# Optimization experiments

Measured on AMD Instinct MI355X. Metric: run time of the kernel, lower is better.

## Reference

```python
import jax, jax.numpy as jnp
import numpy as np

B, L, D, H, PD = 4, 8192, 512, 8, 1
DK = D // H
EPS = 1e-5


def setup_inputs() -> dict:
    root = jax.random.key(0)
    ks = jax.random.split(root, 16)
    s = 0.02
    inp = {
        'query': jax.random.normal(ks[0], (B, L, D), jnp.float32),
        'key': jax.random.normal(ks[1], (B, L, D), jnp.float32),
        'value': jax.random.normal(ks[2], (B, L, D), jnp.float32),
        'pos': jax.random.uniform(ks[3], (B, L, PD), jnp.float32),
        # QKV projections (xavier-ish small + diagonal init, as in _reset_parameters)
        'Wq': s * jax.random.normal(ks[4], (D, D), jnp.float32) + 0.01 * jnp.eye(D),
        'bq': jnp.zeros((D,), jnp.float32),
        'Wk': s * jax.random.normal(ks[5], (D, D), jnp.float32) + 0.01 * jnp.eye(D),
        'bk': jnp.zeros((D,), jnp.float32),
        'Wv': s * jax.random.normal(ks[6], (D, D), jnp.float32) + 0.01 * jnp.eye(D),
        'bv': jnp.zeros((D,), jnp.float32),
        # per-head LayerNorm affine params for K and V: [H, DK]
        'gK': jnp.ones((H, DK), jnp.float32),
        'betaK': jnp.zeros((H, DK), jnp.float32),
        'gV': jnp.ones((H, DK), jnp.float32),
        'betaV': jnp.zeros((H, DK), jnp.float32),
        # output fc: (D + H*PD) -> D
        'fcW': s * jax.random.normal(ks[7], (D, D + H * PD), jnp.float32),
        'fcb': jnp.zeros((D,), jnp.float32),
    }
    return inp


def _proj(x, W, b):
    # [B,L,D] -> [B,H,L,DK]
    return (x @ W.T + b).reshape(B, L, H, DK).transpose(0, 2, 1, 3)


def _head_layernorm(x, g, b):
    # x: [B,H,L,DK]; per-head affine params g,b: [H,DK]; biased variance (torch LN)
    m = x.mean(-1, keepdims=True)
    v = x.var(-1, keepdims=True)
    xn = (x - m) * jax.lax.rsqrt(v + EPS)
    return xn * g[None, :, None, :] + b[None, :, None, :]


def reference(query, key, value, pos, Wq, bq, Wk, bk, Wv, bv,
              gK, betaK, gV, betaV, fcW, fcb):
    q = _proj(query, Wq, bq)
    k = _proj(key, Wk, bk)
    v = _proj(value, Wv, bv)
    k = _head_layernorm(k, gK, betaK)
    v = _head_layernorm(v, gV, betaV)
    # positional concat: pos [B,L,PD] -> [B,H,L,PD], concat on feature dim
    p = jnp.broadcast_to(pos[:, None, :, :], (B, H, L, PD))
    q = jnp.concatenate([p, q], axis=-1)  # [B,H,L,DK+PD]
    k = jnp.concatenate([p, k], axis=-1)
    v = jnp.concatenate([p, v], axis=-1)
    # Galerkin linear attention: (K^T V)/L then Q @ that
    attn = jnp.einsum('bhld,bhle->bhde', k, v) / L  # [B,H,DK+PD,DK+PD]
    out = jnp.einsum('bhld,bhde->bhle', q, attn)    # [B,H,L,DK+PD]
    out = out.transpose(0, 2, 1, 3).reshape(B, L, H * (DK + PD))
    att_output = out @ fcW.T + fcb  # [B,L,D]
    return (att_output, attn)
```

## Files before the change

kernel.cpp:

```cpp
#include <hip/hip_runtime.h>

typedef __attribute__((ext_vector_type(8))) short short8;
typedef __attribute__((ext_vector_type(4))) float f32x4;
typedef __attribute__((ext_vector_type(4))) unsigned short ushort4v;
typedef __attribute__((ext_vector_type(4))) unsigned int uint4v;
typedef unsigned short ushort;
typedef unsigned int uint;

#define B_  4
#define L_  8192
#define D_  512
#define H_  8
#define F_  65
#define CF_ 520
#define CFP_ 544
#define KVS_ 80
#define EPS_ 1e-5f

__device__ __forceinline__ ushort f2b(float f) {
    uint x = __float_as_uint(f);
    uint r = (x + 0x7FFFu + ((x >> 16) & 1u)) >> 16;
    return (ushort)r;
}
__device__ __forceinline__ float b2f(ushort u) {
    return __uint_as_float(((uint)u) << 16);
}

#define GLD16(gptr, sptr) \
    __builtin_amdgcn_global_load_lds((const __attribute__((address_space(1))) void*)(gptr), \
                                     (__attribute__((address_space(3))) void*)(sptr), 16, 0, 0)

__device__ __forceinline__ size_t pk_off(int col, int row) {
    return (size_t)(col >> 5) * 4096 + (size_t)(((col >> 3) & 3) * 1024 + row * 8 + (col & 7));
}

__global__ __launch_bounds__(256)
void cast_w(const float* __restrict__ Wq, const float* __restrict__ Wk,
            const float* __restrict__ Wv, ushort* __restrict__ Wb)
{
    const int g = blockIdx.x * 256 + threadIdx.x;
    const int inner = g & 511;
    const int tileIdx = g >> 9;
    const int w   = inner >> 7;
    const int row = inner & 127;
    const int ks  = tileIdx & 15;
    const int nt  = (tileIdx >> 4) & 3;
    const int z   = tileIdx >> 6;
    const float* __restrict__ src = (z == 0) ? Wq : (z == 1) ? Wk : Wv;
    const float* s = &src[(size_t)(nt * 128 + row) * D_ + ks * 32 + w * 8];
    const float4 f0 = *(const float4*)s;
    const float4 f1 = *(const float4*)(s + 4);
    short8 v;
    v[0] = (short)f2b(f0.x); v[1] = (short)f2b(f0.y);
    v[2] = (short)f2b(f0.z); v[3] = (short)f2b(f0.w);
    v[4] = (short)f2b(f1.x); v[5] = (short)f2b(f1.y);
    v[6] = (short)f2b(f1.z); v[7] = (short)f2b(f1.w);
    *(short8*)&Wb[(size_t)tileIdx * 4096 + inner * 8] = v;
}

__global__ __launch_bounds__(256, 2)
void proj_mfma(const float* __restrict__ Xq, const float* __restrict__ Xk,
               const float* __restrict__ Xv, const ushort* __restrict__ Wb,
               const float* __restrict__ bq, const float* __restrict__ bk,
               const float* __restrict__ bv, const float* __restrict__ pos,
               const float* __restrict__ gK, const float* __restrict__ betaK,
               const float* __restrict__ gV, const float* __restrict__ betaV,
               ushort* __restrict__ Qc, ushort* __restrict__ Kh,
               ushort* __restrict__ Vh)
{
    const int x  = blockIdx.x;
    const int m0 = (((x >> 5) << 3) + (x & 7)) * 128;
    const int n0 = ((x >> 3) & 3) * 128;
    const int z  = blockIdx.y;

    const float*  __restrict__ X    = (z == 0) ? Xq : (z == 1) ? Xk : Xv;
    const float*  __restrict__ bias = (z == 0) ? bq : (z == 1) ? bk : bv;

    const int t  = threadIdx.x;
    const int w  = t >> 6, l = t & 63;
    const int wm = (w >> 1) * 64, wn = (w & 1) * 64;
    const int lg = l >> 4, lm = l & 15;

    __shared__ __align__(16) float sAf[2][4096];
    __shared__ __align__(16) short sB[2][4096];

    f32x4 acc[4][4];
#pragma unroll
    for (int i = 0; i < 4; ++i)
#pragma unroll
        for (int j = 0; j < 4; ++j) acc[i][j] = (f32x4){0.f, 0.f, 0.f, 0.f};

    const int lr = l >> 3;
    const int hg = (l & 7) ^ lr;
    const float* ag[4]; int alo[4];
#pragma unroll
    for (int i = 0; i < 4; ++i) {
        const int row = (w * 4 + i) * 8 + lr;
        ag[i]  = &X[(size_t)(m0 + row) * D_ + hg * 4];
        alo[i] = (w * 4 + i) * 256;
    }

    const ushort* bsrc = Wb + (size_t)((z * 4 + (n0 >> 7)) * 16) * 4096 + w * 1024 + l * 8;
    const int blo0 = w * 1024, blo1 = w * 1024 + 512;

    int a0o[4], a1o[4], bro[4];
#pragma unroll
    for (int i = 0; i < 4; ++i) {
        const int r = wm + i * 16 + lm;
        a0o[i] = r * 32 + (((lg * 2)     ^ (r & 7)) * 4);
        a1o[i] = r * 32 + (((lg * 2 + 1) ^ (r & 7)) * 4);
        bro[i] = lg * 1024 + (wn + i * 16 + lm) * 8;
    }

    auto stage = [&](int ks, int buf) {
#pragma unroll
        for (int i = 0; i < 4; ++i) GLD16(ag[i] + ks * 32, &sAf[buf][alo[i]]);
        GLD16(bsrc + (size_t)ks * 4096,       &sB[buf][blo0]);
        GLD16(bsrc + (size_t)ks * 4096 + 512, &sB[buf][blo1]);
    };

    stage(0, 0);
    int cur = 0;
#pragma unroll
    for (int ks = 0; ks < 16; ++ks) {
        __syncthreads();
        if (ks < 15) stage(ks + 1, cur ^ 1);

        short8 af[4], bfv[4];
#pragma unroll
        for (int i = 0; i < 4; ++i) {
            const f32x4 A0 = *(const f32x4*)&sAf[cur][a0o[i]];
            const f32x4 A1 = *(const f32x4*)&sAf[cur][a1o[i]];
            uint u0, u1, u2, u3;
            asm("v_cvt_pk_bf16_f32 %0, %1, %2" : "=v"(u0) : "v"(A0[0]), "v"(A0[1]));
            asm("v_cvt_pk_bf16_f32 %0, %1, %2" : "=v"(u1) : "v"(A0[2]), "v"(A0[3]));
            asm("v_cvt_pk_bf16_f32 %0, %1, %2" : "=v"(u2) : "v"(A1[0]), "v"(A1[1]));
            asm("v_cvt_pk_bf16_f32 %0, %1, %2" : "=v"(u3) : "v"(A1[2]), "v"(A1[3]));
            union { uint4v u4; short8 s8; } cv;
            cv.u4 = (uint4v){u0, u1, u2, u3};
            af[i]  = cv.s8;
            bfv[i] = *(const short8*)&sB[cur][bro[i]];
        }
#pragma unroll
        for (int mt = 0; mt < 4; ++mt)
#pragma unroll
            for (int nt = 0; nt < 4; ++nt)
                acc[mt][nt] = __builtin_amdgcn_mfma_f32_16x16x32_bf16(
                    af[mt], bfv[nt], acc[mt][nt], 0, 0, 0);

        cur ^= 1;
    }

    const int h = (n0 >> 6) + (w & 1);
    float bvv[4];
#pragma unroll
    for (int nt = 0; nt < 4; ++nt) bvv[nt] = bias[n0 + wn + nt * 16 + lm];

    if (z == 0) {
#pragma unroll
        for (int mt = 0; mt < 4; ++mt) {
#pragma unroll
            for (int r = 0; r < 4; ++r) {
                const int m = m0 + wm + mt * 16 + lg * 4 + r;
                const int mtile = m >> 7, rowin = m & 127;
                ushort* tb = Qc + (size_t)(mtile * 17) * 4096 + rowin * 8;
#pragma unroll
                for (int nt = 0; nt < 4; ++nt) {
                    const int col = h * F_ + 1 + nt * 16 + lm;
                    tb[pk_off(col, 0)] = f2b(acc[mt][nt][r] + bvv[nt]);
                }
                if (lm == 15) {
                    const int col = h * F_;
                    tb[pk_off(col, 0)] = f2b(pos[m]);
                }
                if (h == 7 && lm < 12) {
                    const int wreg = 1 + (lm >> 2);
                    const int e2 = (lm & 3) * 2;
                    *(uint*)&tb[(size_t)16 * 4096 + wreg * 1024 + e2] = 0u;
                }
            }
        }
    } else {
        const float* gp = (z == 1) ? gK : gV;
        const float* bp = (z == 1) ? betaK : betaV;
        ushort* Oh = (z == 1) ? Kh : Vh;
        float gg[4], bb2[4];
#pragma unroll
        for (int nt = 0; nt < 4; ++nt) {
            gg[nt]  = gp[h * 64 + nt * 16 + lm];
            bb2[nt] = bp[h * 64 + nt * 16 + lm];
        }
#pragma unroll
        for (int mt = 0; mt < 4; ++mt) {
#pragma unroll
            for (int r = 0; r < 4; ++r) {
                float v0 = acc[mt][0][r] + bvv[0];
                float v1 = acc[mt][1][r] + bvv[1];
                float v2 = acc[mt][2][r] + bvv[2];
                float v3 = acc[mt][3][r] + bvv[3];
                float s = v0 + v1 + v2 + v3;
                float q = v0 * v0 + v1 * v1 + v2 * v2 + v3 * v3;
                s += __shfl_xor(s, 1); s += __shfl_xor(s, 2);
                s += __shfl_xor(s, 4); s += __shfl_xor(s, 8);
                q += __shfl_xor(q, 1); q += __shfl_xor(q, 2);
                q += __shfl_xor(q, 4); q += __shfl_xor(q, 8);
                const float mean = s * (1.f / 64.f);
                const float var = q * (1.f / 64.f) - mean * mean;
                const float rs = rsqrtf(var + EPS_);
                const int m = m0 + wm + mt * 16 + lg * 4 + r;
                const int bb = m >> 13, ll = m & 8191;
                ushort* row = Oh + ((size_t)(bb * H_ + h) * L_ + ll) * KVS_;
                row[1 + 0 * 16 + lm] = f2b((v0 - mean) * rs * gg[0] + bb2[0]);
                row[1 + 1 * 16 + lm] = f2b((v1 - mean) * rs * gg[1] + bb2[1]);
                row[1 + 2 * 16 + lm] = f2b((v2 - mean) * rs * gg[2] + bb2[2]);
                row[1 + 3 * 16 + lm] = f2b((v3 - mean) * rs * gg[3] + bb2[3]);
                if (lm == 15) row[0] = f2b(pos[m]);
                else          row[F_ + lm] = 0;
            }
        }
    }
}

__global__ __launch_bounds__(256)
void attn_accum(const ushort* __restrict__ Kh, const ushort* __restrict__ Vh,
                float* __restrict__ attn_acc)
{
    const int s = blockIdx.x;
    const int h = blockIdx.y;
    const int b = blockIdx.z;
    const int t = threadIdx.x;

    __shared__ __align__(16) float Ks[64][84];
    __shared__ __align__(16) float Vs[64][84];

    const size_t base = ((size_t)(b * H_ + h) * L_ + s * 512) * KVS_;

    float acc[5][5];
#pragma unroll
    for (int i = 0; i < 5; ++i)
#pragma unroll
        for (int j = 0; j < 5; ++j) acc[i][j] = 0.f;

    const int dg = t / 13, eg = t % 13;
    const bool act = (t < 169);
    const int d0 = dg * 5, e0 = eg * 5;

    for (int c = 0; c < 8; ++c) {
#pragma unroll
        for (int i = 0; i < 3; ++i) {
            const int slot = t + i * 256;
            if (slot < 640) {
                const int r = slot / 10;
                const int cc = (slot - r * 10) * 8;
                const size_t g = base + (size_t)(c * 64 + r) * KVS_ + cc;
                const short8 kv = *(const short8*)(const void*)&Kh[g];
                const short8 vv = *(const short8*)(const void*)&Vh[g];
                float* kd = &Ks[r][cc];
                float* vd = &Vs[r][cc];
#pragma unroll
                for (int e = 0; e < 8; ++e) {
                    kd[e] = b2f((ushort)kv[e]);
                    vd[e] = b2f((ushort)vv[e]);
                }
            }
        }
        __syncthreads();
        if (act) {
#pragma unroll 2
            for (int l = 0; l < 64; ++l) {
                float kf[5], vf[5];
#pragma unroll
                for (int i = 0; i < 5; ++i) kf[i] = Ks[l][d0 + i];
#pragma unroll
                for (int j = 0; j < 5; ++j) vf[j] = Vs[l][e0 + j];
#pragma unroll
                for (int i = 0; i < 5; ++i)
#pragma unroll
                    for (int j = 0; j < 5; ++j)
                        acc[i][j] = fmaf(kf[i], vf[j], acc[i][j]);
            }
        }
        __syncthreads();
    }

    if (act) {
        float* dst = attn_acc + (size_t)(b * H_ + h) * (F_ * F_);
#pragma unroll
        for (int i = 0; i < 5; ++i)
#pragma unroll
            for (int j = 0; j < 5; ++j)
                atomicAdd(&dst[(d0 + i) * F_ + (e0 + j)], acc[i][j]);
    }
}

__global__ __launch_bounds__(256)
void attn_fin_G(const float* __restrict__ attn_acc, const float* __restrict__ fcW,
                float* __restrict__ attn_out, ushort* __restrict__ Gt)
{
    const int nc = blockIdx.x;
    const int h = blockIdx.y;
    const int b = blockIdx.z;
    const int t = threadIdx.x;

    __shared__ float S[F_][F_];
    __shared__ float Wl[64][F_];

    const float inv = 1.0f / (float)L_;
    const float* __restrict__ src = attn_acc + (size_t)(b * H_ + h) * F_ * F_;
    for (int idx = t; idx < F_ * F_; idx += 256) {
        const float v = src[idx] * inv;
        S[idx / F_][idx % F_] = v;
        if (nc == 0) attn_out[(size_t)(b * H_ + h) * F_ * F_ + idx] = v;
    }
    for (int idx = t; idx < 64 * F_; idx += 256) {
        const int j = idx / F_;
        const int e = idx - j * F_;
        Wl[j][e] = fcW[(size_t)(nc * 64 + j) * CF_ + h * F_ + e];
    }
    __syncthreads();

    for (int idx = t; idx < F_ * 64; idx += 256) {
        const int d = idx >> 6;
        const int j = idx & 63;
        float g = 0.f;
#pragma unroll 5
        for (int e = 0; e < F_; ++e) g = fmaf(S[d][e], Wl[j][e], g);
        const int jg = nc * 64 + j;
        const int col = h * F_ + d;
        Gt[(size_t)((b * 4 + (jg >> 7)) * 17) * 4096 + (jg & 127) * 8 + pk_off(col, 0)] = f2b(g);
    }
    if (h == 7) {
        for (int i2 = t; i2 < 64 * 24; i2 += 256) {
            const int j = i2 / 24;
            const int col = CF_ + (i2 % 24);
            const int jg = nc * 64 + j;
            Gt[(size_t)((b * 4 + (jg >> 7)) * 17) * 4096 + (jg & 127) * 8 + pk_off(col, 0)] = 0;
        }
    }
}

__global__ __launch_bounds__(256, 2)
void out_mfma(const ushort* __restrict__ Qc, const ushort* __restrict__ Gt,
              const float* __restrict__ fcb, float* __restrict__ out)
{
    const int x  = blockIdx.x;
    const int m0 = (((x >> 5) << 3) + (x & 7)) * 128;
    const int n0 = ((x >> 3) & 3) * 128;
    const int b  = blockIdx.z;
    const int t  = threadIdx.x;
    const int w  = t >> 6, l = t & 63;
    const int wm = (w >> 1) * 64, wn = (w & 1) * 64;
    const int lg = l >> 4, lm = l & 15;

    __shared__ __align__(16) short sA[2][4096];
    __shared__ __align__(16) short sB[2][4096];

    f32x4 acc[4][4];
#pragma unroll
    for (int i = 0; i < 4; ++i)
#pragma unroll
        for (int j = 0; j < 4; ++j) acc[i][j] = (f32x4){0.f, 0.f, 0.f, 0.f};

    const int mtA = (b * L_ + m0) >> 7;
    const ushort* asrc = Qc + (size_t)(mtA * 17) * 4096 + w * 1024 + l * 8;
    const ushort* bsrc = Gt + (size_t)((b * 4 + (n0 >> 7)) * 17) * 4096 + w * 1024 + l * 8;
    const int lo0 = w * 1024, lo1 = w * 1024 + 512;

    int aro[4], bro[4];
#pragma unroll
    for (int i = 0; i < 4; ++i) {
        aro[i] = lg * 1024 + (wm + i * 16 + lm) * 8;
        bro[i] = lg * 1024 + (wn + i * 16 + lm) * 8;
    }

    auto stage = [&](int ks, int buf) {
        GLD16(asrc + (size_t)ks * 4096,       &sA[buf][lo0]);
        GLD16(asrc + (size_t)ks * 4096 + 512, &sA[buf][lo1]);
        GLD16(bsrc + (size_t)ks * 4096,       &sB[buf][lo0]);
        GLD16(bsrc + (size_t)ks * 4096 + 512, &sB[buf][lo1]);
    };

    stage(0, 0);
    int cur = 0;
#pragma unroll
    for (int ks = 0; ks < 17; ++ks) {
        __syncthreads();
        if (ks < 16) stage(ks + 1, cur ^ 1);

        short8 af[4], bfv[4];
#pragma unroll
        for (int i = 0; i < 4; ++i) {
            af[i]  = *(const short8*)&sA[cur][aro[i]];
            bfv[i] = *(const short8*)&sB[cur][bro[i]];
        }
#pragma unroll
        for (int mt = 0; mt < 4; ++mt)
#pragma unroll
            for (int nt = 0; nt < 4; ++nt)
                acc[mt][nt] = __builtin_amdgcn_mfma_f32_16x16x32_bf16(
                    af[mt], bfv[nt], acc[mt][nt], 0, 0, 0);

        cur ^= 1;
    }

    float bvv[4];
#pragma unroll
    for (int nt = 0; nt < 4; ++nt) bvv[nt] = fcb[n0 + wn + nt * 16 + lm];

#pragma unroll
    for (int mt = 0; mt < 4; ++mt) {
#pragma unroll
        for (int r = 0; r < 4; ++r) {
            const int row = m0 + wm + mt * 16 + lg * 4 + r;
            float* orow = out + ((size_t)b * L_ + row) * D_;
#pragma unroll
            for (int nt = 0; nt < 4; ++nt)
                orow[n0 + wn + nt * 16 + lm] = acc[mt][nt][r] + bvv[nt];
        }
    }
}

extern "C" void kernel_launch(void* const* d_in, const int* in_sizes, int n_in,
                              void* d_out, int out_size, void* d_ws, size_t ws_size,
                              hipStream_t stream)
{
    const float* query = (const float*)d_in[0];
    const float* key   = (const float*)d_in[1];
    const float* value = (const float*)d_in[2];
    const float* pos   = (const float*)d_in[3];
    const float* Wq    = (const float*)d_in[4];
    const float* bq    = (const float*)d_in[5];
    const float* Wk    = (const float*)d_in[6];
    const float* bk    = (const float*)d_in[7];
    const float* Wv    = (const float*)d_in[8];
    const float* bv    = (const float*)d_in[9];
    const float* gK    = (const float*)d_in[10];
    const float* betaK = (const float*)d_in[11];
    const float* gV    = (const float*)d_in[12];
    const float* betaV = (const float*)d_in[13];
    const float* fcW   = (const float*)d_in[14];
    const float* fcb   = (const float*)d_in[15];

    char* ws = (char*)d_ws;
    ushort* Qc       = (ushort*)(ws + 0);
    ushort* Kh       = (ushort*)(ws + 35651584);
    ushort* Vh       = (ushort*)(ws + 77594624);
    ushort* Wb       = (ushort*)(ws + 119537664);
    float*  attn_acc = (float*) (ws + 121110528);
    ushort* Gt       = (ushort*)(ws + 121651328);

    float* att_out  = (float*)d_out;
    float* attn_out = att_out + 16777216;

    hipMemsetAsync(attn_acc, 0, (size_t)135200 * sizeof(float), stream);

    cast_w<<<dim3(384), 256, 0, stream>>>(Wq, Wk, Wv, Wb);

    proj_mfma<<<dim3(1024, 3), 256, 0, stream>>>(
        query, key, value, Wb, bq, bk, bv, pos,
        gK, betaK, gV, betaV, Qc, Kh, Vh);

    attn_accum<<<dim3(16, 8, 4), 256, 0, stream>>>(Kh, Vh, attn_acc);

    attn_fin_G<<<dim3(8, 8, 4), 256, 0, stream>>>(attn_acc, fcW, attn_out, Gt);

    out_mfma<<<dim3(256, 1, 4), 256, 0, stream>>>(Qc, Gt, fcb, att_out);
}
```

Measured before the change: 498.8 us.

## Widen projection and output GEMM tiles to 128x256 to halve A re-reads

Both proj_mfma and out_mfma now compute 128x256 output tiles per block, with each wave holding a 64x128 accumulator (4x8 MFMA tiles), and the grids are halved to match. This halves how often the fp32 activation A tile is read from global memory and converted to bf16, which is a large share of the memory traffic in the projection. In exchange, accumulator registers double, B-tile LDS doubles, and there are fewer blocks, which risks spills and lower occupancy under launch_bounds(256,2). The Q-pad zeroing condition and the per-head LayerNorm are adjusted so each wave handles two heads.

```diff
diff --git a/kernel.cpp b/kernel.cpp
--- a/kernel.cpp
+++ b/kernel.cpp
@@ -69,8 +69,9 @@
                ushort* __restrict__ Vh)
 {
     const int x  = blockIdx.x;
-    const int m0 = (((x >> 5) << 3) + (x & 7)) * 128;
-    const int n0 = ((x >> 3) & 3) * 128;
+    const int m0 = (((x >> 4) << 3) + (x & 7)) * 128;
+    const int nh = (x >> 3) & 1;
+    const int n0 = nh * 256;
     const int z  = blockIdx.y;
 
     const float*  __restrict__ X    = (z == 0) ? Xq : (z == 1) ? Xk : Xv;
@@ -78,17 +79,17 @@
 
     const int t  = threadIdx.x;
     const int w  = t >> 6, l = t & 63;
-    const int wm = (w >> 1) * 64, wn = (w & 1) * 64;
+    const int wm = (w >> 1) * 64, wn = (w & 1) * 128;
     const int lg = l >> 4, lm = l & 15;
 
     __shared__ __align__(16) float sAf[2][4096];
-    __shared__ __align__(16) short sB[2][4096];
-
-    f32x4 acc[4][4];
+    __shared__ __align__(16) short sB[2][8192];
+
+    f32x4 acc[4][8];
 #pragma unroll
     for (int i = 0; i < 4; ++i)
 #pragma unroll
-        for (int j = 0; j < 4; ++j) acc[i][j] = (f32x4){0.f, 0.f, 0.f, 0.f};
+        for (int j = 0; j < 8; ++j) acc[i][j] = (f32x4){0.f, 0.f, 0.f, 0.f};
 
     const int lr = l >> 3;
     const int hg = (l & 7) ^ lr;
@@ -100,23 +101,30 @@
         alo[i] = (w * 4 + i) * 256;
     }
 
-    const ushort* bsrc = Wb + (size_t)((z * 4 + (n0 >> 7)) * 16) * 4096 + w * 1024 + l * 8;
+    const ushort* bsrc0 = Wb + (size_t)((z * 4 + nh * 2) * 16) * 4096 + w * 1024 + l * 8;
+    const ushort* bsrc1 = bsrc0 + (size_t)16 * 4096;
     const int blo0 = w * 1024, blo1 = w * 1024 + 512;
 
-    int a0o[4], a1o[4], bro[4];
+    int a0o[4], a1o[4], bro[8];
 #pragma unroll
     for (int i = 0; i < 4; ++i) {
         const int r = wm + i * 16 + lm;
         a0o[i] = r * 32 + (((lg * 2)     ^ (r & 7)) * 4);
         a1o[i] = r * 32 + (((lg * 2 + 1) ^ (r & 7)) * 4);
-        bro[i] = lg * 1024 + (wn + i * 16 + lm) * 8;
+    }
+#pragma unroll
+    for (int i = 0; i < 8; ++i) {
+        const int col = wn + i * 16 + lm;
+        bro[i] = (col >> 7) * 4096 + lg * 1024 + (col & 127) * 8;
     }
 
     auto stage = [&](int ks, int buf) {
 #pragma unroll
         for (int i = 0; i < 4; ++i) GLD16(ag[i] + ks * 32, &sAf[buf][alo[i]]);
-        GLD16(bsrc + (size_t)ks * 4096,       &sB[buf][blo0]);
-        GLD16(bsrc + (size_t)ks * 4096 + 512, &sB[buf][blo1]);
+        GLD16(bsrc0 + (size_t)ks * 4096,       &sB[buf][blo0]);
+        GLD16(bsrc0 + (size_t)ks * 4096 + 512, &sB[buf][blo1]);
+        GLD16(bsrc1 + (size_t)ks * 4096,       &sB[buf][4096 + blo0]);
+        GLD16(bsrc1 + (size_t)ks * 4096 + 512, &sB[buf][4096 + blo1]);
     };
 
     stage(0, 0);
@@ -126,7 +134,7 @@
         __syncthreads();
         if (ks < 15) stage(ks + 1, cur ^ 1);
 
-        short8 af[4], bfv[4];
+        short8 af[4], bfv[8];
 #pragma unroll
         for (int i = 0; i < 4; ++i) {
             const f32x4 A0 = *(const f32x4*)&sAf[cur][a0o[i]];
@@ -138,23 +146,24 @@
             asm("v_cvt_pk_bf16_f32 %0, %1, %2" : "=v"(u3) : "v"(A1[2]), "v"(A1[3]));
             union { uint4v u4; short8 s8; } cv;
             cv.u4 = (uint4v){u0, u1, u2, u3};
-            af[i]  = cv.s8;
-            bfv[i] = *(const short8*)&sB[cur][bro[i]];
-        }
+            af[i] = cv.s8;
+        }
+#pragma unroll
+        for (int i = 0; i < 8; ++i) bfv[i] = *(const short8*)&sB[cur][bro[i]];
 #pragma unroll
         for (int mt = 0; mt < 4; ++mt)
 #pragma unroll
-            for (int nt = 0; nt < 4; ++nt)
+            for (int nt = 0; nt < 8; ++nt)
                 acc[mt][nt] = __builtin_amdgcn_mfma_f32_16x16x32_bf16(
                     af[mt], bfv[nt], acc[mt][nt], 0, 0, 0);
 
         cur ^= 1;
     }
 
-    const int h = (n0 >> 6) + (w & 1);
-    float bvv[4];
-#pragma unroll
-    for (int nt = 0; nt < 4; ++nt) bvv[nt] = bias[n0 + wn + nt * 16 + lm];
+    const int h0 = (n0 + wn) >> 6;
+    float bvv[8];
+#pragma unroll
+    for (int nt = 0; nt < 8; ++nt) bvv[nt] = bias[n0 + wn + nt * 16 + lm];
 
     if (z == 0) {
 #pragma unroll
@@ -165,15 +174,15 @@
                 const int mtile = m >> 7, rowin = m & 127;
                 ushort* tb = Qc + (size_t)(mtile * 17) * 4096 + rowin * 8;
 #pragma unroll
-                for (int nt = 0; nt < 4; ++nt) {
-                    const int col = h * F_ + 1 + nt * 16 + lm;
+                for (int nt = 0; nt < 8; ++nt) {
+                    const int col = (h0 + (nt >> 2)) * F_ + 1 + (nt & 3) * 16 + lm;
                     tb[pk_off(col, 0)] = f2b(acc[mt][nt][r] + bvv[nt]);
                 }
                 if (lm == 15) {
-                    const int col = h * F_;
-                    tb[pk_off(col, 0)] = f2b(pos[m]);
+                    tb[pk_off(h0 * F_, 0)]       = f2b(pos[m]);
+                    tb[pk_off((h0 + 1) * F_, 0)] = f2b(pos[m]);
                 }
-                if (h == 7 && lm < 12) {
+                if (h0 == 6 && lm < 12) {
                     const int wreg = 1 + (lm >> 2);
                     const int e2 = (lm & 3) * 2;
                     *(uint*)&tb[(size_t)16 * 4096 + wreg * 1024 + e2] = 0u;
@@ -184,38 +193,43 @@
         const float* gp = (z == 1) ? gK : gV;
         const float* bp = (z == 1) ? betaK : betaV;
         ushort* Oh = (z == 1) ? Kh : Vh;
-        float gg[4], bb2[4];
-#pragma unroll
-        for (int nt = 0; nt < 4; ++nt) {
-            gg[nt]  = gp[h * 64 + nt * 16 + lm];
-            bb2[nt] = bp[h * 64 + nt * 16 + lm];
+        float gg[8], bb2[8];
+#pragma unroll
+        for (int nt = 0; nt < 8; ++nt) {
+            const int idx = (h0 + (nt >> 2)) * 64 + (nt & 3) * 16 + lm;
+            gg[nt]  = gp[idx];
+            bb2[nt] = bp[idx];
         }
 #pragma unroll
         for (int mt = 0; mt < 4; ++mt) {
 #pragma unroll
             for (int r = 0; r < 4; ++r) {
-                float v0 = acc[mt][0][r] + bvv[0];
-                float v1 = acc[mt][1][r] + bvv[1];
-                float v2 = acc[mt][2][r] + bvv[2];
-                float v3 = acc[mt][3][r] + bvv[3];
-                float s = v0 + v1 + v2 + v3;
-                float q = v0 * v0 + v1 * v1 + v2 * v2 + v3 * v3;
-                s += __shfl_xor(s, 1); s += __shfl_xor(s, 2);
-                s += __shfl_xor(s, 4); s += __shfl_xor(s, 8);
-                q += __shfl_xor(q, 1); q += __shfl_xor(q, 2);
-                q += __shfl_xor(q, 4); q += __shfl_xor(q, 8);
-                const float mean = s * (1.f / 64.f);
-                const float var = q * (1.f / 64.f) - mean * mean;
-                const float rs = rsqrtf(var + EPS_);
                 const int m = m0 + wm + mt * 16 + lg * 4 + r;
                 const int bb = m >> 13, ll = m & 8191;
-                ushort* row = Oh + ((size_t)(bb * H_ + h) * L_ + ll) * KVS_;
-                row[1 + 0 * 16 + lm] = f2b((v0 - mean) * rs * gg[0] + bb2[0]);
-                row[1 + 1 * 16 + lm] = f2b((v1 - mean) * rs * gg[1] + bb2[1]);
-                row[1 + 2 * 16 + lm] = f2b((v2 - mean) * rs * gg[2] + bb2[2]);
-                row[1 + 3 * 16 + lm] = f2b((v3 - mean) * rs * gg[3] + bb2[3]);
-                if (lm == 15) row[0] = f2b(pos[m]);
-                else          row[F_ + lm] = 0;
+#pragma unroll
+                for (int g = 0; g < 2; ++g) {
+                    const float v0 = acc[mt][g * 4 + 0][r] + bvv[g * 4 + 0];
+                    const float v1 = acc[mt][g * 4 + 1][r] + bvv[g * 4 + 1];
+                    const float v2 = acc[mt][g * 4 + 2][r] + bvv[g * 4 + 2];
+                    const float v3 = acc[mt][g * 4 + 3][r] + bvv[g * 4 + 3];
+                    float s = v0 + v1 + v2 + v3;
+                    float q = v0 * v0 + v1 * v1 + v2 * v2 + v3 * v3;
+                    s += __shfl_xor(s, 1); s += __shfl_xor(s, 2);
+                    s += __shfl_xor(s, 4); s += __shfl_xor(s, 8);
+                    q += __shfl_xor(q, 1); q += __shfl_xor(q, 2);
+                    q += __shfl_xor(q, 4); q += __shfl_xor(q, 8);
+                    const float mean = s * (1.f / 64.f);
+                    const float var = q * (1.f / 64.f) - mean * mean;
+                    const float rs = rsqrtf(var + EPS_);
+                    const int h = h0 + g;
+                    ushort* row = Oh + ((size_t)(bb * H_ + h) * L_ + ll) * KVS_;
+                    row[1 + 0 * 16 + lm] = f2b((v0 - mean) * rs * gg[g * 4 + 0] + bb2[g * 4 + 0]);
+                    row[1 + 1 * 16 + lm] = f2b((v1 - mean) * rs * gg[g * 4 + 1] + bb2[g * 4 + 1]);
+                    row[1 + 2 * 16 + lm] = f2b((v2 - mean) * rs * gg[g * 4 + 2] + bb2[g * 4 + 2]);
+                    row[1 + 3 * 16 + lm] = f2b((v3 - mean) * rs * gg[g * 4 + 3] + bb2[g * 4 + 3]);
+                    if (lm == 15) row[0] = f2b(pos[m]);
+                    else          row[F_ + lm] = 0;
+                }
             }
         }
     }
@@ -344,40 +358,47 @@
               const float* __restrict__ fcb, float* __restrict__ out)
 {
     const int x  = blockIdx.x;
-    const int m0 = (((x >> 5) << 3) + (x & 7)) * 128;
-    const int n0 = ((x >> 3) & 3) * 128;
+    const int m0 = (((x >> 4) << 3) + (x & 7)) * 128;
+    const int nh = (x >> 3) & 1;
+    const int n0 = nh * 256;
     const int b  = blockIdx.z;
     const int t  = threadIdx.x;
     const int w  = t >> 6, l = t & 63;
-    const int wm = (w >> 1) * 64, wn = (w & 1) * 64;
+    const int wm = (w >> 1) * 64, wn = (w & 1) * 128;
     const int lg = l >> 4, lm = l & 15;
 
     __shared__ __align__(16) short sA[2][4096];
-    __shared__ __align__(16) short sB[2][4096];
-
-    f32x4 acc[4][4];
+    __shared__ __align__(16) short sB[2][8192];
+
+    f32x4 acc[4][8];
 #pragma unroll
     for (int i = 0; i < 4; ++i)
 #pragma unroll
-        for (int j = 0; j < 4; ++j) acc[i][j] = (f32x4){0.f, 0.f, 0.f, 0.f};
+        for (int j = 0; j < 8; ++j) acc[i][j] = (f32x4){0.f, 0.f, 0.f, 0.f};
 
     const int mtA = (b * L_ + m0) >> 7;
-    const ushort* asrc = Qc + (size_t)(mtA * 17) * 4096 + w * 1024 + l * 8;
-    const ushort* bsrc = Gt + (size_t)((b * 4 + (n0 >> 7)) * 17) * 4096 + w * 1024 + l * 8;
+    const ushort* asrc  = Qc + (size_t)(mtA * 17) * 4096 + w * 1024 + l * 8;
+    const ushort* bsrc0 = Gt + (size_t)((b * 4 + nh * 2) * 17) * 4096 + w * 1024 + l * 8;
+    const ushort* bsrc1 = bsrc0 + (size_t)17 * 4096;
     const int lo0 = w * 1024, lo1 = w * 1024 + 512;
 
-    int aro[4], bro[4];
-#pragma unroll
-    for (int i = 0; i < 4; ++i) {
+    int aro[4], bro[8];
+#pragma unroll
+    for (int i = 0; i < 4; ++i)
         aro[i] = lg * 1024 + (wm + i * 16 + lm) * 8;
-        bro[i] = lg * 1024 + (wn + i * 16 + lm) * 8;
+#pragma unroll
+    for (int i = 0; i < 8; ++i) {
+        const int col = wn + i * 16 + lm;
+        bro[i] = (col >> 7) * 4096 + lg * 1024 + (col & 127) * 8;
     }
 
     auto stage = [&](int ks, int buf) {
-        GLD16(asrc + (size_t)ks * 4096,       &sA[buf][lo0]);
-        GLD16(asrc + (size_t)ks * 4096 + 512, &sA[buf][lo1]);
-        GLD16(bsrc + (size_t)ks * 4096,       &sB[buf][lo0]);
-        GLD16(bsrc + (size_t)ks * 4096 + 512, &sB[buf][lo1]);
+        GLD16(asrc  + (size_t)ks * 4096,       &sA[buf][lo0]);
+        GLD16(asrc  + (size_t)ks * 4096 + 512, &sA[buf][lo1]);
+        GLD16(bsrc0 + (size_t)ks * 4096,       &sB[buf][lo0]);
+        GLD16(bsrc0 + (size_t)ks * 4096 + 512, &sB[buf][lo1]);
+        GLD16(bsrc1 + (size_t)ks * 4096,       &sB[buf][4096 + lo0]);
+        GLD16(bsrc1 + (size_t)ks * 4096 + 512, &sB[buf][4096 + lo1]);
     };
 
     stage(0, 0);
@@ -387,25 +408,24 @@
         __syncthreads();
         if (ks < 16) stage(ks + 1, cur ^ 1);
 
-        short8 af[4], bfv[4];
-#pragma unroll
-        for (int i = 0; i < 4; ++i) {
-            af[i]  = *(const short8*)&sA[cur][aro[i]];
-            bfv[i] = *(const short8*)&sB[cur][bro[i]];
-        }
+        short8 af[4], bfv[8];
+#pragma unroll
+        for (int i = 0; i < 4; ++i) af[i]  = *(const short8*)&sA[cur][aro[i]];
+#pragma unroll
+        for (int i = 0; i < 8; ++i) bfv[i] = *(const short8*)&sB[cur][bro[i]];
 #pragma unroll
         for (int mt = 0; mt < 4; ++mt)
 #pragma unroll
-            for (int nt = 0; nt < 4; ++nt)
+            for (int nt = 0; nt < 8; ++nt)
                 acc[mt][nt] = __builtin_amdgcn_mfma_f32_16x16x32_bf16(
                     af[mt], bfv[nt], acc[mt][nt], 0, 0, 0);
 
         cur ^= 1;
     }
 
-    float bvv[4];
-#pragma unroll
-    for (int nt = 0; nt < 4; ++nt) bvv[nt] = fcb[n0 + wn + nt * 16 + lm];
+    float bvv[8];
+#pragma unroll
+    for (int nt = 0; nt < 8; ++nt) bvv[nt] = fcb[n0 + wn + nt * 16 + lm];
 
 #pragma unroll
     for (int mt = 0; mt < 4; ++mt) {
@@ -414,7 +434,7 @@
             const int row = m0 + wm + mt * 16 + lg * 4 + r;
             float* orow = out + ((size_t)b * L_ + row) * D_;
 #pragma unroll
-            for (int nt = 0; nt < 4; ++nt)
+            for (int nt = 0; nt < 8; ++nt)
                 orow[n0 + wn + nt * 16 + lm] = acc[mt][nt][r] + bvv[nt];
         }
     }
@@ -456,7 +476,7 @@
 
     cast_w<<<dim3(384), 256, 0, stream>>>(Wq, Wk, Wv, Wb);
 
-    proj_mfma<<<dim3(1024, 3), 256, 0, stream>>>(
+    proj_mfma<<<dim3(512, 3), 256, 0, stream>>>(
         query, key, value, Wb, bq, bk, bv, pos,
         gK, betaK, gV, betaV, Qc, Kh, Vh);
 
@@ -464,5 +484,5 @@
 
     attn_fin_G<<<dim3(8, 8, 4), 256, 0, stream>>>(attn_acc, fcW, attn_out, Gt);
 
-    out_mfma<<<dim3(256, 1, 4), 256, 0, stream>>>(Qc, Gt, fcb, att_out);
-}
+    out_mfma<<<dim3(128, 1, 4), 256, 0, stream>>>(Qc, Gt, fcb, att_out);
+}
```

Result: faster. 460.3 us (-7.7%).
